# Kernel optimization log

Hardware: AMD Instinct MI355X
Metric: run time of the kernel (lower is better)

## Reference

```python
import jax, jax.numpy as jnp
import numpy as np

B, S, T = 128, 1024, 512
VOCAB, E, HE, HD, ATT = 1000, 128, 64, 66, 32


def setup_inputs() -> dict:
    key = jax.random.key(0)
    ks = jax.random.split(key, 14)
    p = lambda k, shape: (jax.random.normal(k, shape, dtype=jnp.float32) * 0.05)
    return {
        'x': jax.random.randint(ks[0], (B, S), 0, VOCAB, dtype=jnp.int32),
        'c': jax.random.normal(ks[1], (B, T), dtype=jnp.float32),
        'emb': p(ks[2], (VOCAB, E)),
        'enc_Wih': p(ks[3], (4 * HE, E)),
        'enc_Whh': p(ks[4], (4 * HE, HE)),
        'enc_b': p(ks[5], (4 * HE,)),
        'att_fc_W': p(ks[6], (HE, E)),
        'att_fc_b': p(ks[7], (HE,)),
        'att_w_W': p(ks[8], (ATT, HE)),
        'att_w_b': p(ks[9], (ATT,)),
        'dec_Wih': p(ks[10], (4 * HD, ATT)),
        'dec_Whh': p(ks[11], (4 * HD, HD)),
        'dec_b': p(ks[12], (4 * HD,)),
        'fin_W': p(ks[13], (E, HD)),
        'fin_b': jnp.zeros((E,), dtype=jnp.float32),
    }


def _lstm_seq(xs, W_ih, W_hh, b, H):
    # xs: [B, S, in]; PyTorch gate order i, f, g, o
    bsz = xs.shape[0]
    gx = jnp.einsum('bsi,gi->bsg', xs, W_ih) + b  # [B,S,4H]

    def step(carry, g_t):
        h, c = carry
        g = g_t + h @ W_hh.T
        i, f, gg, o = jnp.split(g, 4, axis=-1)
        c = jax.nn.sigmoid(f) * c + jax.nn.sigmoid(i) * jnp.tanh(gg)
        h = jax.nn.sigmoid(o) * jnp.tanh(c)
        return (h, c), h

    h0 = jnp.zeros((bsz, H), xs.dtype)
    (_, _), hs = jax.lax.scan(step, (h0, h0), jnp.swapaxes(gx, 0, 1))
    return jnp.swapaxes(hs, 0, 1)  # [B,S,H]


def reference(x, c, emb, enc_Wih, enc_Whh, enc_b, att_fc_W, att_fc_b,
              att_w_W, att_w_b, dec_Wih, dec_Whh, dec_b, fin_W, fin_b):
    # encoder: embed + LSTM, returns full sequence of hidden states [B,S,64]
    enc = _lstm_seq(emb[x], enc_Wih, enc_Whh, enc_b, HE)
    bsz, steps = x.shape[0], c.shape[1]
    # initial decoder input: embedding of token 0, broadcast over batch
    x0 = jnp.broadcast_to(emb[0], (bsz, E))
    h0 = jnp.zeros((bsz, HD), enc.dtype)

    def step(carry, _):
        xemb, h, cc = carry
        # attend(a=xemb, A=enc)
        a = xemb @ att_fc_W.T + att_fc_b                     # [B,64]
        A = a[:, None, :] * enc                              # [B,S,64]
        alpha = jax.nn.softmax(
            jnp.tanh(jnp.einsum('bse,ae->bsa', A, att_w_W) + att_w_b),
            axis=-1)                                         # [B,S,32]
        beta = alpha.sum(axis=1)                             # [B,32]
        # decoder LSTM cell (one timestep)
        g = beta @ dec_Wih.T + h @ dec_Whh.T + dec_b
        i, f, gg, o = jnp.split(g, 4, axis=-1)
        cc = jax.nn.sigmoid(f) * cc + jax.nn.sigmoid(i) * jnp.tanh(gg)
        h = jax.nn.sigmoid(o) * jnp.tanh(cc)
        xemb = h @ fin_W.T + fin_b                           # feed back via final_fc
        return (xemb, h, cc), h

    _, hs = jax.lax.scan(step, (x0, h0, h0), None, length=steps)
    return jnp.swapaxes(hs, 0, 1)  # [B,T,66]
```

## Files before the change

### kernel.cpp

```cpp
#include <hip/hip_runtime.h>
#include <hip/hip_bf16.h>

#define kB 128
#define kS 1024
#define kT 512
#define kV 1000
#define kE 128
#define kHE 64
#define kHD 66
#define kATT 32
#define kGE 256
#define kGD 264

typedef __attribute__((ext_vector_type(4))) float f32x4;
typedef __attribute__((ext_vector_type(8))) short bf16x8;
typedef __attribute__((ext_vector_type(8))) unsigned short u16x8;

__device__ __forceinline__ unsigned short f2bf(float f) {
  unsigned int u = __builtin_bit_cast(unsigned int, f);
  u += 0x7FFFu + ((u >> 16) & 1u);
  return (unsigned short)(u >> 16);
}
__device__ __forceinline__ float rcp_(float x) { return __builtin_amdgcn_rcpf(x); }
__device__ __forceinline__ float fsig(float x)  { return rcp_(1.0f + __expf(-x)); }
__device__ __forceinline__ float ftanh(float x) { return 1.0f - 2.0f * rcp_(1.0f + __expf(2.0f * x)); }
__device__ __forceinline__ float fexp2(float z) {
#if __has_builtin(__builtin_amdgcn_exp2f)
  return __builtin_amdgcn_exp2f(z);
#else
  return __expf(z * 0.6931471805599453f);
#endif
}
__device__ __forceinline__ const unsigned short* launder_us(const unsigned short* p) {
  asm volatile("" : "+s"(p));
  return p;
}

__global__ __launch_bounds__(256) void prep_kernel(
    const float* __restrict__ emb, const float* __restrict__ enc_Wih,
    const float* __restrict__ enc_b, const float* __restrict__ enc_Whh,
    const float* __restrict__ att_fc_W, const float* __restrict__ att_fc_b,
    const float* __restrict__ att_w_W,
    const float* __restrict__ fin_W, const float* __restrict__ fin_b,
    const float* __restrict__ dec_Wih, const float* __restrict__ dec_Whh,
    const float* __restrict__ dec_b,
    float* __restrict__ embW, unsigned short* __restrict__ decF,
    unsigned short* __restrict__ encF, unsigned short* __restrict__ afF,
    float* __restrict__ wregF, float* __restrict__ dbias,
    float* __restrict__ abias, float* __restrict__ ainit) {
  int bid = blockIdx.x, tid = threadIdx.x;
  if (bid < kV) {
    float acc = enc_b[tid];
    const float* er = emb + bid * kE;
    const float* wr = enc_Wih + tid * kE;
    for (int e = 0; e < kE; ++e) acc += er[e] * wr[e];
    embW[bid * kGE + tid] = acc;
  } else if (bid == kV) {
    for (int i = tid; i < 17 * 4 * 64 * 8; i += 256) {
      int jj = i & 7, lane = (i >> 3) & 63, ts = i >> 9;
      int tile = ts >> 2, ks = ts & 3;
      int j = tile * 16 + (lane & 15);
      int k = ks * 32 + ((lane >> 4) << 3) + jj;
      float v = 0.f;
      if (j < kGD) {
        if (k < 32) v = dec_Wih[j * kATT + k];
        else if (k < 98) v = dec_Whh[j * kHD + (k - 32)];
      }
      decF[i] = f2bf(v);
    }
  } else if (bid == kV + 1) {
    for (int i = tid; i < 16 * 2 * 64 * 8; i += 256) {
      int jj = i & 7, lane = (i >> 3) & 63, ts = i >> 9;
      int tile = ts >> 1, ks = ts & 1;
      int j = tile * 16 + (lane & 15);
      int k = ks * 32 + ((lane >> 4) << 3) + jj;
      encF[i] = f2bf(enc_Whh[j * kHE + k]);
    }
  } else if (bid == kV + 2) {
    for (int i = tid; i < 4 * 3 * 64 * 8; i += 256) {
      int jj = i & 7, lane = (i >> 3) & 63, ts = i >> 9;
      int tile = ts / 3, ks = ts - tile * 3;
      int aidx = tile * 16 + (lane & 15);
      int m = ks * 32 + ((lane >> 4) << 3) + jj;
      float v = 0.f;
      if (m < kHD)
        for (int e = 0; e < kE; ++e) v += att_fc_W[aidx * kE + e] * fin_W[e * kHD + m];
      afF[i] = f2bf(v);
    }
  } else if (bid == kV + 3) {
    for (int i = tid; i < 8 * 64 * 4; i += 256) {
      int c = i & 3, lane = (i >> 2) & 63, jq = i >> 8;
      int half = jq & 1, kc = (jq >> 1) & 1, mt = jq >> 2;
      wregF[i] = att_w_W[(mt * 16 + (lane & 15)) * kHE + kc * 32 + ((lane >> 4) << 3) + half * 4 + c];
    }
  } else if (bid == kV + 4) {
    for (int j = tid; j < kGD; j += 256) {
      float s = 0.f;
      for (int m = 0; m < kATT; ++m) s += dec_Wih[j * kATT + m];
      dbias[j] = dec_b[j] + 32.0f * s;
    }
  } else {
    if (tid < kHE) {
      float acc = att_fc_b[tid];
      for (int e = 0; e < kE; ++e) acc += att_fc_W[tid * kE + e] * fin_b[e];
      abias[tid] = acc;
    } else if (tid < 2 * kHE) {
      int a = tid - kHE;
      float acc = att_fc_b[a];
      for (int e = 0; e < kE; ++e) acc += emb[e] * att_fc_W[a * kE + e];
      ainit[a] = acc;
    }
  }
}

__global__ __launch_bounds__(256)
__attribute__((amdgpu_waves_per_eu(1, 1)))
void enc_kernel(
    const int* __restrict__ x, const float* __restrict__ embW,
    const unsigned short* __restrict__ encF, float* __restrict__ out) {
  __shared__ struct __align__(16) {
    unsigned short xe[64];
    float gbuf[kGE];
    int toks[kS];
  } sm;
  const int b = blockIdx.x, t = threadIdx.x, lane = t & 63, wv = t >> 6;

  for (int i = t; i < kS; i += 256) sm.toks[i] = x[b * kS + i];
  if (t < 64) sm.xe[t] = 0;

  u16x8 eQ[4][2];
  #pragma unroll
  for (int q = 0; q < 4; ++q)
    #pragma unroll
    for (int ks = 0; ks < 2; ++ks)
      eQ[q][ks] = *(const u16x8*)&encF[(((wv * 4 + q) * 2 + ks) * 64 + lane) * 8];
  __syncthreads();

  float gx0 = 0, gx1 = 0, gx2 = 0, gx3 = 0;
  if (lane < 16) {
    int tok = sm.toks[0];
    gx0 = embW[tok * kGE + wv * 64 + 0 + lane];
    gx1 = embW[tok * kGE + wv * 64 + 16 + lane];
    gx2 = embW[tok * kGE + wv * 64 + 32 + lane];
    gx3 = embW[tok * kGE + wv * 64 + 48 + lane];
  }
  float cE = 0.0f;
  unsigned short* eg = (unsigned short*)(out + (size_t)b * (kT * kHD));

  for (int s = 0; s < kS; ++s) {
    union { u16x8 u; bf16x8 v; } xa0, xa1;
    xa0.u = *(const u16x8*)&sm.xe[(lane >> 4) << 3];
    xa1.u = *(const u16x8*)&sm.xe[32 + ((lane >> 4) << 3)];
    float gn0 = 0, gn1 = 0, gn2 = 0, gn3 = 0;
    int tokn = sm.toks[(s + 1 < kS) ? (s + 1) : s];
    if (lane < 16) {
      gn0 = embW[tokn * kGE + wv * 64 + 0 + lane];
      gn1 = embW[tokn * kGE + wv * 64 + 16 + lane];
      gn2 = embW[tokn * kGE + wv * 64 + 32 + lane];
      gn3 = embW[tokn * kGE + wv * 64 + 48 + lane];
    }
    f32x4 z = {0.f, 0.f, 0.f, 0.f};
    f32x4 a0 = __builtin_amdgcn_mfma_f32_16x16x32_bf16(xa0.v, eQ[0][0], z, 0, 0, 0);
    a0 = __builtin_amdgcn_mfma_f32_16x16x32_bf16(xa1.v, eQ[0][1], a0, 0, 0, 0);
    f32x4 a1 = __builtin_amdgcn_mfma_f32_16x16x32_bf16(xa0.v, eQ[1][0], z, 0, 0, 0);
    a1 = __builtin_amdgcn_mfma_f32_16x16x32_bf16(xa1.v, eQ[1][1], a1, 0, 0, 0);
    f32x4 a2 = __builtin_amdgcn_mfma_f32_16x16x32_bf16(xa0.v, eQ[2][0], z, 0, 0, 0);
    a2 = __builtin_amdgcn_mfma_f32_16x16x32_bf16(xa1.v, eQ[2][1], a2, 0, 0, 0);
    f32x4 a3 = __builtin_amdgcn_mfma_f32_16x16x32_bf16(xa0.v, eQ[3][0], z, 0, 0, 0);
    a3 = __builtin_amdgcn_mfma_f32_16x16x32_bf16(xa1.v, eQ[3][1], a3, 0, 0, 0);
    if (lane < 16) {
      sm.gbuf[wv * 64 + 0 + lane]  = a0[0] + gx0;
      sm.gbuf[wv * 64 + 16 + lane] = a1[0] + gx1;
      sm.gbuf[wv * 64 + 32 + lane] = a2[0] + gx2;
      sm.gbuf[wv * 64 + 48 + lane] = a3[0] + gx3;
    }
    __syncthreads();
    if (t < 64) {
      float gi = sm.gbuf[t], gf = sm.gbuf[64 + t], gg = sm.gbuf[128 + t], go = sm.gbuf[192 + t];
      cE = fsig(gf) * cE + fsig(gi) * ftanh(gg);
      float h = fsig(go) * ftanh(cE);
      unsigned short hb = f2bf(h);
      sm.xe[t] = hb;
      eg[s * 64 + ((((t >> 3) ^ (s & 7)) << 3) | (t & 7))] = hb;
    }
    __syncthreads();
    gx0 = gn0; gx1 = gn1; gx2 = gn2; gx3 = gn3;
  }
}

struct __align__(16) DSm {
  unsigned short enc[kS * kHE];
  float wregL[8 * 64 * 4];
  unsigned short xv[128];
  float aa[64];
  float betaW[16][32];
  float gbuf[kGD];
};

union U8 { u16x8 u; bf16x8 v; };

__global__ __launch_bounds__(1024)
void dec_kernel(
    const float* __restrict__ att_w_b,
    const unsigned short* __restrict__ decF, const unsigned short* __restrict__ afF,
    const float* __restrict__ wregF_ws, const float* __restrict__ dbias_ws,
    const float* __restrict__ abias_ws, const float* __restrict__ ainit_ws,
    float* __restrict__ out) {
  __shared__ DSm sm;
  const int b = blockIdx.x, t = threadIdx.x, lane = t & 63, wv = t >> 6;
  const int lr = lane & 15, g = lane >> 4;

  {
    const u16x8* src = (const u16x8*)(out + (size_t)b * (kT * kHD));
    u16x8* dst = (u16x8*)sm.enc;
    #pragma unroll
    for (int i = 0; i < 8; ++i) dst[t + i * 1024] = src[t + i * 1024];
  }
  for (int i = t; i < 8 * 64 * 4; i += 1024) sm.wregL[i] = wregF_ws[i];

  f32x4 wb0, wb1;
  #pragma unroll
  for (int r = 0; r < 4; ++r) {
    wb0[r] = att_w_b[g * 4 + r];
    wb1[r] = att_w_b[16 + g * 4 + r];
  }
  float dbr = (lane < 16) ? dbias_ws[wv * 16 + lane] : 0.f;
  float dbr2 = (wv == 8 && lane < 8) ? dbias_ws[256 + lane] : 0.f;
  float abr = (wv < 4 && lane < 16) ? abias_ws[wv * 16 + lane] : 0.f;

  if (t < 128) sm.xv[t] = 0;
  if (t < 64) sm.aa[t] = ainit_ws[t];
  float cD = 0.0f;
  __syncthreads();

  const int sbase = wv * 64;
  for (int step = 0; step < kT; ++step) {
    U8 dq0, dq1, dq2, dq3, tq0, tq1, tq2, tq3, aq0, aq1, aq2;
    {
      const f32x4* aap = (const f32x4*)sm.aa;
      const f32x4* wrl = (const f32x4*)sm.wregL;
      bf16x8 af[2][2];
      #pragma unroll
      for (int kc = 0; kc < 2; ++kc) {
        f32x4 a0v = aap[kc * 8 + g * 2];
        f32x4 a1v = aap[kc * 8 + g * 2 + 1];
        #pragma unroll
        for (int mt = 0; mt < 2; ++mt) {
          f32x4 w0 = wrl[((mt * 2 + kc) * 2 + 0) * 64 + lane];
          f32x4 w1 = wrl[((mt * 2 + kc) * 2 + 1) * 64 + lane];
          union { bf16x8 v; __hip_bfloat162 h2[4]; } tmp;
          tmp.h2[0] = __float22bfloat162_rn(make_float2(w0.x * a0v.x, w0.y * a0v.y));
          tmp.h2[1] = __float22bfloat162_rn(make_float2(w0.z * a0v.z, w0.w * a0v.w));
          tmp.h2[2] = __float22bfloat162_rn(make_float2(w1.x * a1v.x, w1.y * a1v.y));
          tmp.h2[3] = __float22bfloat162_rn(make_float2(w1.z * a1v.z, w1.w * a1v.w));
          af[mt][kc] = tmp.v;
        }
      }
      float betaAcc[2][4] = {};
      float amax = 0.0f;
      #pragma unroll
      for (int nt = 0; nt < 4; ++nt) {
        int s = sbase + nt * 16 + lr;
        int sw = s & 7;
        U8 e0, e1;
        e0.u = *(const u16x8*)&sm.enc[s * kHE + ((g ^ sw) << 3)];
        e1.u = *(const u16x8*)&sm.enc[s * kHE + (((4 + g) ^ sw) << 3)];
        f32x4 acc0 = __builtin_amdgcn_mfma_f32_16x16x32_bf16(af[0][0], e0.v, wb0, 0, 0, 0);
        acc0 = __builtin_amdgcn_mfma_f32_16x16x32_bf16(af[0][1], e1.v, acc0, 0, 0, 0);
        f32x4 acc1 = __builtin_amdgcn_mfma_f32_16x16x32_bf16(af[1][0], e0.v, wb1, 0, 0, 0);
        acc1 = __builtin_amdgcn_mfma_f32_16x16x32_bf16(af[1][1], e1.v, acc1, 0, 0, 0);
        float u0[4], u1[4], dsum = 0.f;
        #pragma unroll
        for (int r = 0; r < 4; ++r) {
          float x0 = acc0[r], x1 = acc1[r];
          amax = fmaxf(amax, fmaxf(__builtin_fabsf(x0), __builtin_fabsf(x1)));
          u0[r] = fexp2(x0 * __builtin_fmaf(x0 * x0, -0.48089835f, 1.44269504f));
          u1[r] = fexp2(x1 * __builtin_fmaf(x1 * x1, -0.48089835f, 1.44269504f));
          dsum += u0[r] + u1[r];
        }
        dsum += __shfl_xor(dsum, 16);
        dsum += __shfl_xor(dsum, 32);
        float invd = rcp_(dsum);
        #pragma unroll
        for (int r = 0; r < 4; ++r) {
          betaAcc[0][r] += u0[r] * invd;
          betaAcc[1][r] += u1[r] * invd;
        }
      }
      if (__builtin_expect(__any(amax > 0.35f), 0)) {
        #pragma unroll
        for (int mt = 0; mt < 2; ++mt)
          #pragma unroll
          for (int r = 0; r < 4; ++r) betaAcc[mt][r] = 0.f;
        for (int nt = 0; nt < 4; ++nt) {
          int s = sbase + nt * 16 + lr;
          int sw = s & 7;
          U8 e0, e1;
          e0.u = *(const u16x8*)&sm.enc[s * kHE + ((g ^ sw) << 3)];
          e1.u = *(const u16x8*)&sm.enc[s * kHE + (((4 + g) ^ sw) << 3)];
          f32x4 acc0 = __builtin_amdgcn_mfma_f32_16x16x32_bf16(af[0][0], e0.v, wb0, 0, 0, 0);
          acc0 = __builtin_amdgcn_mfma_f32_16x16x32_bf16(af[0][1], e1.v, acc0, 0, 0, 0);
          f32x4 acc1 = __builtin_amdgcn_mfma_f32_16x16x32_bf16(af[1][0], e0.v, wb1, 0, 0, 0);
          acc1 = __builtin_amdgcn_mfma_f32_16x16x32_bf16(af[1][1], e1.v, acc1, 0, 0, 0);
          float u0[4], u1[4], dsum = 0.f;
          for (int r = 0; r < 4; ++r) {
            u0[r] = __expf(tanhf(acc0[r]));
            u1[r] = __expf(tanhf(acc1[r]));
            dsum += u0[r] + u1[r];
          }
          dsum += __shfl_xor(dsum, 16);
          dsum += __shfl_xor(dsum, 32);
          float invd = rcp_(dsum);
          for (int r = 0; r < 4; ++r) {
            betaAcc[0][r] += u0[r] * invd;
            betaAcc[1][r] += u1[r] * invd;
          }
        }
      }
      {
        const unsigned short* dFp = launder_us(decF);
        dq0.u = *(const u16x8*)&dFp[((wv * 4 + 0) * 64 + lane) * 8];
        dq1.u = *(const u16x8*)&dFp[((wv * 4 + 1) * 64 + lane) * 8];
        dq2.u = *(const u16x8*)&dFp[((wv * 4 + 2) * 64 + lane) * 8];
        dq3.u = *(const u16x8*)&dFp[((wv * 4 + 3) * 64 + lane) * 8];
        if (wv == 8) {
          tq0.u = *(const u16x8*)&dFp[((16 * 4 + 0) * 64 + lane) * 8];
          tq1.u = *(const u16x8*)&dFp[((16 * 4 + 1) * 64 + lane) * 8];
          tq2.u = *(const u16x8*)&dFp[((16 * 4 + 2) * 64 + lane) * 8];
          tq3.u = *(const u16x8*)&dFp[((16 * 4 + 3) * 64 + lane) * 8];
        }
        if (wv < 4) {
          const unsigned short* aFp = launder_us(afF);
          aq0.u = *(const u16x8*)&aFp[((wv * 3 + 0) * 64 + lane) * 8];
          aq1.u = *(const u16x8*)&aFp[((wv * 3 + 1) * 64 + lane) * 8];
          aq2.u = *(const u16x8*)&aFp[((wv * 3 + 2) * 64 + lane) * 8];
        }
      }
      #pragma unroll
      for (int mt = 0; mt < 2; ++mt)
        #pragma unroll
        for (int r = 0; r < 4; ++r) {
          float v = betaAcc[mt][r];
          v += __shfl_xor(v, 1);
          v += __shfl_xor(v, 2);
          v += __shfl_xor(v, 4);
          v += __shfl_xor(v, 8);
          if (lr == 0) sm.betaW[wv][mt * 16 + g * 4 + r] = v;
        }
    }
    __syncthreads();
    if (t < kATT) {
      float sb = 0.f;
      #pragma unroll
      for (int w = 0; w < 16; ++w) sb += sm.betaW[w][t];
      sm.xv[t] = f2bf(sb - 32.0f);
    }
    __syncthreads();
    {
      U8 xg0, xg1, xg2, xg3;
      xg0.u = *(const u16x8*)&sm.xv[(g << 3)];
      xg1.u = *(const u16x8*)&sm.xv[32 + (g << 3)];
      xg2.u = *(const u16x8*)&sm.xv[64 + (g << 3)];
      xg3.u = *(const u16x8*)&sm.xv[96 + (g << 3)];
      f32x4 z = {0.f, 0.f, 0.f, 0.f};
      f32x4 ga = __builtin_amdgcn_mfma_f32_16x16x32_bf16(xg0.v, dq0.v, z, 0, 0, 0);
      ga = __builtin_amdgcn_mfma_f32_16x16x32_bf16(xg1.v, dq1.v, ga, 0, 0, 0);
      ga = __builtin_amdgcn_mfma_f32_16x16x32_bf16(xg2.v, dq2.v, ga, 0, 0, 0);
      ga = __builtin_amdgcn_mfma_f32_16x16x32_bf16(xg3.v, dq3.v, ga, 0, 0, 0);
      if (lane < 16) sm.gbuf[wv * 16 + lane] = ga[0] + dbr;
      if (wv == 8) {
        f32x4 gb = __builtin_amdgcn_mfma_f32_16x16x32_bf16(xg0.v, tq0.v, z, 0, 0, 0);
        gb = __builtin_amdgcn_mfma_f32_16x16x32_bf16(xg1.v, tq1.v, gb, 0, 0, 0);
        gb = __builtin_amdgcn_mfma_f32_16x16x32_bf16(xg2.v, tq2.v, gb, 0, 0, 0);
        gb = __builtin_amdgcn_mfma_f32_16x16x32_bf16(xg3.v, tq3.v, gb, 0, 0, 0);
        if (lane < 8) sm.gbuf[256 + lane] = gb[0] + dbr2;
      }
    }
    __syncthreads();
    if (t < kHD) {
      float gi = sm.gbuf[t], gf = sm.gbuf[kHD + t], gg = sm.gbuf[2 * kHD + t], go = sm.gbuf[3 * kHD + t];
      cD = fsig(gf) * cD + fsig(gi) * ftanh(gg);
      float h = fsig(go) * ftanh(cD);
      sm.xv[32 + t] = f2bf(h);
      out[((size_t)b * kT + step) * kHD + t] = h;
    }
    __syncthreads();
    if (wv < 4) {
      U8 y0, y1, y2;
      y0.u = *(const u16x8*)&sm.xv[32 + (g << 3)];
      y1.u = *(const u16x8*)&sm.xv[64 + (g << 3)];
      y2.u = *(const u16x8*)&sm.xv[96 + (g << 3)];
      f32x4 z = {0.f, 0.f, 0.f, 0.f};
      f32x4 aacc = __builtin_amdgcn_mfma_f32_16x16x32_bf16(y0.v, aq0.v, z, 0, 0, 0);
      aacc = __builtin_amdgcn_mfma_f32_16x16x32_bf16(y1.v, aq1.v, aacc, 0, 0, 0);
      aacc = __builtin_amdgcn_mfma_f32_16x16x32_bf16(y2.v, aq2.v, aacc, 0, 0, 0);
      if (lane < 16) sm.aa[wv * 16 + lane] = aacc[0] + abr;
    }
    __syncthreads();
  }
}

extern "C" void kernel_launch(void* const* d_in, const int* in_sizes, int n_in,
                              void* d_out, int out_size, void* d_ws, size_t ws_size,
                              hipStream_t stream) {
  const int*   x        = (const int*)d_in[0];
  const float* emb      = (const float*)d_in[2];
  const float* enc_Wih  = (const float*)d_in[3];
  const float* enc_Whh  = (const float*)d_in[4];
  const float* enc_b    = (const float*)d_in[5];
  const float* att_fc_W = (const float*)d_in[6];
  const float* att_fc_b = (const float*)d_in[7];
  const float* att_w_W  = (const float*)d_in[8];
  const float* att_w_b  = (const float*)d_in[9];
  const float* dec_Wih  = (const float*)d_in[10];
  const float* dec_Whh  = (const float*)d_in[11];
  const float* dec_b    = (const float*)d_in[12];
  const float* fin_W    = (const float*)d_in[13];
  const float* fin_b    = (const float*)d_in[14];
  float* out = (float*)d_out;

  float* embW = (float*)d_ws;
  unsigned short* decF = (unsigned short*)(embW + kV * kGE);
  unsigned short* encF = decF + 17 * 4 * 64 * 8;
  unsigned short* afF  = encF + 16 * 2 * 64 * 8;
  float* wregF = (float*)(afF + 4 * 3 * 64 * 8);
  float* dbias = wregF + 8 * 64 * 4;
  float* abias = dbias + kGD;
  float* ainit = abias + kHE;

  prep_kernel<<<dim3(kV + 6), dim3(256), 0, stream>>>(
      emb, enc_Wih, enc_b, enc_Whh, att_fc_W, att_fc_b, att_w_W, fin_W, fin_b,
      dec_Wih, dec_Whh, dec_b, embW, decF, encF, afF, wregF, dbias, abias, ainit);
  enc_kernel<<<dim3(kB), dim3(256), 0, stream>>>(x, embW, encF, out);
  dec_kernel<<<dim3(kB), dim3(1024), 0, stream>>>(
      att_w_b, decF, afF, wregF, dbias, abias, ainit, out);
}
```

Baseline: 3.488 ms.

## Halve decoder block to 512 threads and cut per-step barriers

Runs the decoder with 512 threads per block, so each wave covers 128 sequence positions and two or three gate tiles. The gate K dimension shrinks from four slices to three by handling the last two hidden units (64, 65) as scalar FMAs with weights staged in LDS. The cross-wave beta reduction now uses DPP and LDS atomics instead of a separate reduce phase, which removes one barrier per step. The attention-fc weights and biases also move to LDS, and wave 0 both finishes the LSTM cell and computes the next attention vector. Fewer waves per block means less parallel work in the attention phase, and LDS atomics add contention.

```diff
diff --git a/kernel.cpp b/kernel.cpp
--- a/kernel.cpp
+++ b/kernel.cpp
@@ -34,6 +34,17 @@
 __device__ __forceinline__ const unsigned short* launder_us(const unsigned short* p) {
   asm volatile("" : "+s"(p));
   return p;
+}
+__device__ __forceinline__ float dpp_red16(float v) {
+  int x = __builtin_bit_cast(int, v);
+  v += __builtin_bit_cast(float, __builtin_amdgcn_update_dpp(0, x, 0xB1, 0xf, 0xf, true));
+  x = __builtin_bit_cast(int, v);
+  v += __builtin_bit_cast(float, __builtin_amdgcn_update_dpp(0, x, 0x4E, 0xf, 0xf, true));
+  x = __builtin_bit_cast(int, v);
+  v += __builtin_bit_cast(float, __builtin_amdgcn_update_dpp(0, x, 0x124, 0xf, 0xf, true));
+  x = __builtin_bit_cast(int, v);
+  v += __builtin_bit_cast(float, __builtin_amdgcn_update_dpp(0, x, 0x128, 0xf, 0xf, true));
+  return v;
 }
 
 __global__ __launch_bounds__(256) void prep_kernel(
@@ -47,6 +58,7 @@
     float* __restrict__ embW, unsigned short* __restrict__ decF,
     unsigned short* __restrict__ encF, unsigned short* __restrict__ afF,
     float* __restrict__ wregF, float* __restrict__ dbias,
+    float* __restrict__ wh64, float* __restrict__ wh65,
     float* __restrict__ abias, float* __restrict__ ainit) {
   int bid = blockIdx.x, tid = threadIdx.x;
   if (bid < kV) {
@@ -56,15 +68,15 @@
     for (int e = 0; e < kE; ++e) acc += er[e] * wr[e];
     embW[bid * kGE + tid] = acc;
   } else if (bid == kV) {
-    for (int i = tid; i < 17 * 4 * 64 * 8; i += 256) {
+    for (int i = tid; i < 17 * 3 * 64 * 8; i += 256) {
       int jj = i & 7, lane = (i >> 3) & 63, ts = i >> 9;
-      int tile = ts >> 2, ks = ts & 3;
+      int tile = ts / 3, ks = ts - tile * 3;
       int j = tile * 16 + (lane & 15);
       int k = ks * 32 + ((lane >> 4) << 3) + jj;
       float v = 0.f;
       if (j < kGD) {
         if (k < 32) v = dec_Wih[j * kATT + k];
-        else if (k < 98) v = dec_Whh[j * kHD + (k - 32)];
+        else v = dec_Whh[j * kHD + (k - 32)];
       }
       decF[i] = f2bf(v);
     }
@@ -98,6 +110,8 @@
       float s = 0.f;
       for (int m = 0; m < kATT; ++m) s += dec_Wih[j * kATT + m];
       dbias[j] = dec_b[j] + 32.0f * s;
+      wh64[j] = dec_Whh[j * kHD + 64];
+      wh65[j] = dec_Whh[j * kHD + 65];
     }
   } else {
     if (tid < kHE) {
@@ -191,19 +205,26 @@
 struct __align__(16) DSm {
   unsigned short enc[kS * kHE];
   float wregL[8 * 64 * 4];
-  unsigned short xv[128];
+  unsigned short afL[4 * 3 * 64 * 8];
+  float dbL[kGD];
+  float wh64L[kGD];
+  float wh65L[kGD];
+  float absL[64];
   float aa[64];
-  float betaW[16][32];
+  float beta[32];
+  unsigned short xv[160];
   float gbuf[kGD];
+  float hh2[2];
 };
 
 union U8 { u16x8 u; bf16x8 v; };
 
-__global__ __launch_bounds__(1024)
+__global__ __launch_bounds__(512, 2)
 void dec_kernel(
     const float* __restrict__ att_w_b,
     const unsigned short* __restrict__ decF, const unsigned short* __restrict__ afF,
     const float* __restrict__ wregF_ws, const float* __restrict__ dbias_ws,
+    const float* __restrict__ wh64_ws, const float* __restrict__ wh65_ws,
     const float* __restrict__ abias_ws, const float* __restrict__ ainit_ws,
     float* __restrict__ out) {
   __shared__ DSm sm;
@@ -214,9 +235,19 @@
     const u16x8* src = (const u16x8*)(out + (size_t)b * (kT * kHD));
     u16x8* dst = (u16x8*)sm.enc;
     #pragma unroll
-    for (int i = 0; i < 8; ++i) dst[t + i * 1024] = src[t + i * 1024];
-  }
-  for (int i = t; i < 8 * 64 * 4; i += 1024) sm.wregL[i] = wregF_ws[i];
+    for (int i = 0; i < 16; ++i) dst[t + i * 512] = src[t + i * 512];
+  }
+  ((f32x4*)sm.wregL)[t] = ((const f32x4*)wregF_ws)[t];
+  for (int i = t; i < 768; i += 512) ((u16x8*)sm.afL)[i] = ((const u16x8*)afF)[i];
+  for (int i = t; i < kGD; i += 512) {
+    sm.dbL[i] = dbias_ws[i];
+    sm.wh64L[i] = wh64_ws[i];
+    sm.wh65L[i] = wh65_ws[i];
+  }
+  if (t < 64) { sm.absL[t] = abias_ws[t]; sm.aa[t] = ainit_ws[t]; }
+  if (t < 32) sm.beta[t] = 0.f;
+  if (t < 160) sm.xv[t] = 0;
+  if (t < 2) sm.hh2[t] = 0.f;
 
   f32x4 wb0, wb1;
   #pragma unroll
@@ -224,18 +255,15 @@
     wb0[r] = att_w_b[g * 4 + r];
     wb1[r] = att_w_b[16 + g * 4 + r];
   }
-  float dbr = (lane < 16) ? dbias_ws[wv * 16 + lane] : 0.f;
-  float dbr2 = (wv == 8 && lane < 8) ? dbias_ws[256 + lane] : 0.f;
-  float abr = (wv < 4 && lane < 16) ? abias_ws[wv * 16 + lane] : 0.f;
-
-  if (t < 128) sm.xv[t] = 0;
-  if (t < 64) sm.aa[t] = ainit_ws[t];
-  float cD = 0.0f;
+  float cD = 0.0f, cD2 = 0.0f;
   __syncthreads();
 
-  const int sbase = wv * 64;
+  const int sbase = wv * 128;
+  const int tileA = wv, tileB = wv + 8;
+  const bool has3 = (wv == 7);
+
   for (int step = 0; step < kT; ++step) {
-    U8 dq0, dq1, dq2, dq3, tq0, tq1, tq2, tq3, aq0, aq1, aq2;
+    U8 qa[3], qb[3], qc[3];
     {
       const f32x4* aap = (const f32x4*)sm.aa;
       const f32x4* wrl = (const f32x4*)sm.wregL;
@@ -259,7 +287,7 @@
       float betaAcc[2][4] = {};
       float amax = 0.0f;
       #pragma unroll
-      for (int nt = 0; nt < 4; ++nt) {
+      for (int nt = 0; nt < 8; ++nt) {
         int s = sbase + nt * 16 + lr;
         int sw = s & 7;
         U8 e0, e1;
@@ -292,7 +320,7 @@
         for (int mt = 0; mt < 2; ++mt)
           #pragma unroll
           for (int r = 0; r < 4; ++r) betaAcc[mt][r] = 0.f;
-        for (int nt = 0; nt < 4; ++nt) {
+        for (int nt = 0; nt < 8; ++nt) {
           int s = sbase + nt * 16 + lr;
           int sw = s & 7;
           U8 e0, e1;
@@ -319,82 +347,93 @@
       }
       {
         const unsigned short* dFp = launder_us(decF);
-        dq0.u = *(const u16x8*)&dFp[((wv * 4 + 0) * 64 + lane) * 8];
-        dq1.u = *(const u16x8*)&dFp[((wv * 4 + 1) * 64 + lane) * 8];
-        dq2.u = *(const u16x8*)&dFp[((wv * 4 + 2) * 64 + lane) * 8];
-        dq3.u = *(const u16x8*)&dFp[((wv * 4 + 3) * 64 + lane) * 8];
-        if (wv == 8) {
-          tq0.u = *(const u16x8*)&dFp[((16 * 4 + 0) * 64 + lane) * 8];
-          tq1.u = *(const u16x8*)&dFp[((16 * 4 + 1) * 64 + lane) * 8];
-          tq2.u = *(const u16x8*)&dFp[((16 * 4 + 2) * 64 + lane) * 8];
-          tq3.u = *(const u16x8*)&dFp[((16 * 4 + 3) * 64 + lane) * 8];
-        }
-        if (wv < 4) {
-          const unsigned short* aFp = launder_us(afF);
-          aq0.u = *(const u16x8*)&aFp[((wv * 3 + 0) * 64 + lane) * 8];
-          aq1.u = *(const u16x8*)&aFp[((wv * 3 + 1) * 64 + lane) * 8];
-          aq2.u = *(const u16x8*)&aFp[((wv * 3 + 2) * 64 + lane) * 8];
+        #pragma unroll
+        for (int ks = 0; ks < 3; ++ks) {
+          qa[ks].u = *(const u16x8*)&dFp[((tileA * 3 + ks) * 64 + lane) * 8];
+          qb[ks].u = *(const u16x8*)&dFp[((tileB * 3 + ks) * 64 + lane) * 8];
+        }
+        if (has3) {
+          #pragma unroll
+          for (int ks = 0; ks < 3; ++ks)
+            qc[ks].u = *(const u16x8*)&dFp[((16 * 3 + ks) * 64 + lane) * 8];
         }
       }
       #pragma unroll
       for (int mt = 0; mt < 2; ++mt)
         #pragma unroll
         for (int r = 0; r < 4; ++r) {
-          float v = betaAcc[mt][r];
-          v += __shfl_xor(v, 1);
-          v += __shfl_xor(v, 2);
-          v += __shfl_xor(v, 4);
-          v += __shfl_xor(v, 8);
-          if (lr == 0) sm.betaW[wv][mt * 16 + g * 4 + r] = v;
-        }
-    }
-    __syncthreads();
-    if (t < kATT) {
-      float sb = 0.f;
-      #pragma unroll
-      for (int w = 0; w < 16; ++w) sb += sm.betaW[w][t];
-      sm.xv[t] = f2bf(sb - 32.0f);
+          float v = dpp_red16(betaAcc[mt][r]);
+          if (lr == 0) atomicAdd(&sm.beta[mt * 16 + g * 4 + r], v);
+        }
     }
     __syncthreads();
     {
-      U8 xg0, xg1, xg2, xg3;
-      xg0.u = *(const u16x8*)&sm.xv[(g << 3)];
+      const f32x4* pb = (const f32x4*)sm.beta;
+      f32x4 b0 = pb[g * 2], b1 = pb[g * 2 + 1];
+      union { bf16x8 v; __hip_bfloat162 h2[4]; } bfr;
+      bfr.h2[0] = __float22bfloat162_rn(make_float2(b0.x - 32.f, b0.y - 32.f));
+      bfr.h2[1] = __float22bfloat162_rn(make_float2(b0.z - 32.f, b0.w - 32.f));
+      bfr.h2[2] = __float22bfloat162_rn(make_float2(b1.x - 32.f, b1.y - 32.f));
+      bfr.h2[3] = __float22bfloat162_rn(make_float2(b1.z - 32.f, b1.w - 32.f));
+      U8 xg1, xg2;
       xg1.u = *(const u16x8*)&sm.xv[32 + (g << 3)];
       xg2.u = *(const u16x8*)&sm.xv[64 + (g << 3)];
-      xg3.u = *(const u16x8*)&sm.xv[96 + (g << 3)];
+      float hh0 = sm.hh2[0], hh1 = sm.hh2[1];
       f32x4 z = {0.f, 0.f, 0.f, 0.f};
-      f32x4 ga = __builtin_amdgcn_mfma_f32_16x16x32_bf16(xg0.v, dq0.v, z, 0, 0, 0);
-      ga = __builtin_amdgcn_mfma_f32_16x16x32_bf16(xg1.v, dq1.v, ga, 0, 0, 0);
-      ga = __builtin_amdgcn_mfma_f32_16x16x32_bf16(xg2.v, dq2.v, ga, 0, 0, 0);
-      ga = __builtin_amdgcn_mfma_f32_16x16x32_bf16(xg3.v, dq3.v, ga, 0, 0, 0);
-      if (lane < 16) sm.gbuf[wv * 16 + lane] = ga[0] + dbr;
-      if (wv == 8) {
-        f32x4 gb = __builtin_amdgcn_mfma_f32_16x16x32_bf16(xg0.v, tq0.v, z, 0, 0, 0);
-        gb = __builtin_amdgcn_mfma_f32_16x16x32_bf16(xg1.v, tq1.v, gb, 0, 0, 0);
-        gb = __builtin_amdgcn_mfma_f32_16x16x32_bf16(xg2.v, tq2.v, gb, 0, 0, 0);
-        gb = __builtin_amdgcn_mfma_f32_16x16x32_bf16(xg3.v, tq3.v, gb, 0, 0, 0);
-        if (lane < 8) sm.gbuf[256 + lane] = gb[0] + dbr2;
+      f32x4 ga = __builtin_amdgcn_mfma_f32_16x16x32_bf16(bfr.v, qa[0].v, z, 0, 0, 0);
+      ga = __builtin_amdgcn_mfma_f32_16x16x32_bf16(xg1.v, qa[1].v, ga, 0, 0, 0);
+      ga = __builtin_amdgcn_mfma_f32_16x16x32_bf16(xg2.v, qa[2].v, ga, 0, 0, 0);
+      f32x4 gb = __builtin_amdgcn_mfma_f32_16x16x32_bf16(bfr.v, qb[0].v, z, 0, 0, 0);
+      gb = __builtin_amdgcn_mfma_f32_16x16x32_bf16(xg1.v, qb[1].v, gb, 0, 0, 0);
+      gb = __builtin_amdgcn_mfma_f32_16x16x32_bf16(xg2.v, qb[2].v, gb, 0, 0, 0);
+      if (lane < 16) {
+        int ja = tileA * 16 + lane;
+        sm.gbuf[ja] = ga[0] + sm.dbL[ja] + sm.wh64L[ja] * hh0 + sm.wh65L[ja] * hh1;
+        int jb = tileB * 16 + lane;
+        sm.gbuf[jb] = gb[0] + sm.dbL[jb] + sm.wh64L[jb] * hh0 + sm.wh65L[jb] * hh1;
+      }
+      if (has3) {
+        f32x4 gc = __builtin_amdgcn_mfma_f32_16x16x32_bf16(bfr.v, qc[0].v, z, 0, 0, 0);
+        gc = __builtin_amdgcn_mfma_f32_16x16x32_bf16(xg1.v, qc[1].v, gc, 0, 0, 0);
+        gc = __builtin_amdgcn_mfma_f32_16x16x32_bf16(xg2.v, qc[2].v, gc, 0, 0, 0);
+        if (lane < 8) {
+          int jc = 256 + lane;
+          sm.gbuf[jc] = gc[0] + sm.dbL[jc] + sm.wh64L[jc] * hh0 + sm.wh65L[jc] * hh1;
+        }
       }
     }
     __syncthreads();
-    if (t < kHD) {
-      float gi = sm.gbuf[t], gf = sm.gbuf[kHD + t], gg = sm.gbuf[2 * kHD + t], go = sm.gbuf[3 * kHD + t];
+    if (wv == 0) {
+      float gi = sm.gbuf[lane], gf = sm.gbuf[66 + lane], gg = sm.gbuf[132 + lane], go = sm.gbuf[198 + lane];
       cD = fsig(gf) * cD + fsig(gi) * ftanh(gg);
       float h = fsig(go) * ftanh(cD);
-      sm.xv[32 + t] = f2bf(h);
-      out[((size_t)b * kT + step) * kHD + t] = h;
-    }
-    __syncthreads();
-    if (wv < 4) {
+      sm.xv[32 + lane] = f2bf(h);
+      out[((size_t)b * kT + step) * kHD + lane] = h;
+      if (lane < 2) {
+        float gi2 = sm.gbuf[64 + lane], gf2 = sm.gbuf[130 + lane], gg2 = sm.gbuf[196 + lane], go2 = sm.gbuf[262 + lane];
+        cD2 = fsig(gf2) * cD2 + fsig(gi2) * ftanh(gg2);
+        float h2 = fsig(go2) * ftanh(cD2);
+        sm.xv[96 + lane] = f2bf(h2);
+        sm.hh2[lane] = h2;
+        out[((size_t)b * kT + step) * kHD + 64 + lane] = h2;
+      }
       U8 y0, y1, y2;
       y0.u = *(const u16x8*)&sm.xv[32 + (g << 3)];
       y1.u = *(const u16x8*)&sm.xv[64 + (g << 3)];
       y2.u = *(const u16x8*)&sm.xv[96 + (g << 3)];
       f32x4 z = {0.f, 0.f, 0.f, 0.f};
-      f32x4 aacc = __builtin_amdgcn_mfma_f32_16x16x32_bf16(y0.v, aq0.v, z, 0, 0, 0);
-      aacc = __builtin_amdgcn_mfma_f32_16x16x32_bf16(y1.v, aq1.v, aacc, 0, 0, 0);
-      aacc = __builtin_amdgcn_mfma_f32_16x16x32_bf16(y2.v, aq2.v, aacc, 0, 0, 0);
-      if (lane < 16) sm.aa[wv * 16 + lane] = aacc[0] + abr;
+      #pragma unroll
+      for (int tt = 0; tt < 4; ++tt) {
+        U8 f0, f1, f2;
+        f0.u = *(const u16x8*)&sm.afL[((tt * 3 + 0) * 64 + lane) * 8];
+        f1.u = *(const u16x8*)&sm.afL[((tt * 3 + 1) * 64 + lane) * 8];
+        f2.u = *(const u16x8*)&sm.afL[((tt * 3 + 2) * 64 + lane) * 8];
+        f32x4 acc = __builtin_amdgcn_mfma_f32_16x16x32_bf16(y0.v, f0.v, z, 0, 0, 0);
+        acc = __builtin_amdgcn_mfma_f32_16x16x32_bf16(y1.v, f1.v, acc, 0, 0, 0);
+        acc = __builtin_amdgcn_mfma_f32_16x16x32_bf16(y2.v, f2.v, acc, 0, 0, 0);
+        if (lane < 16) sm.aa[tt * 16 + lane] = acc[0] + sm.absL[tt * 16 + lane];
+      }
+      if (lane < 32) sm.beta[lane] = 0.f;
     }
     __syncthreads();
   }
@@ -421,17 +460,20 @@
 
   float* embW = (float*)d_ws;
   unsigned short* decF = (unsigned short*)(embW + kV * kGE);
-  unsigned short* encF = decF + 17 * 4 * 64 * 8;
+  unsigned short* encF = decF + 17 * 3 * 64 * 8;
   unsigned short* afF  = encF + 16 * 2 * 64 * 8;
   float* wregF = (float*)(afF + 4 * 3 * 64 * 8);
   float* dbias = wregF + 8 * 64 * 4;
-  float* abias = dbias + kGD;
+  float* wh64  = dbias + kGD;
+  float* wh65  = wh64 + kGD;
+  float* abias = wh65 + kGD;
   float* ainit = abias + kHE;
 
   prep_kernel<<<dim3(kV + 6), dim3(256), 0, stream>>>(
       emb, enc_Wih, enc_b, enc_Whh, att_fc_W, att_fc_b, att_w_W, fin_W, fin_b,
-      dec_Wih, dec_Whh, dec_b, embW, decF, encF, afF, wregF, dbias, abias, ainit);
+      dec_Wih, dec_Whh, dec_b, embW, decF, encF, afF, wregF, dbias, wh64, wh65,
+      abias, ainit);
   enc_kernel<<<dim3(kB), dim3(256), 0, stream>>>(x, embW, encF, out);
-  dec_kernel<<<dim3(kB), dim3(1024), 0, stream>>>(
-      att_w_b, decF, afF, wregF, dbias, abias, ainit, out);
-}
+  dec_kernel<<<dim3(kB), dim3(512), 0, stream>>>(
+      att_w_b, decF, afF, wregF, dbias, wh64, wh65, abias, ainit, out);
+}
```

New measurement: 2.867 ms. 1.22x faster.
